# Kernel tuning notes

Hardware: AMD Instinct MI355X
Metric: run time of the kernel (lower is better)

Reference implementation:

```python
import jax, jax.numpy as jnp
import numpy as np

LEAKY_SLOPE = 0.2
LN_EPS = 1e-5


def _gat_layer(x, W, attn, concat):
    # x: (N, in_dim), W: (in_dim, H*D), attn: (H, 2*D)
    N = x.shape[0]
    H, two_d = attn.shape
    D = two_d // 2
    Wx = (x @ W).reshape(N, H, D)
    # (cat([src, tgt]) * attn).sum(-1) decomposes exactly into src/tgt dot products
    e_src = jnp.einsum('nhd,hd->nh', Wx, attn[:, :D])   # score contribution of node i
    e_tgt = jnp.einsum('nhd,hd->nh', Wx, attn[:, D:])   # score contribution of node j
    e = jax.nn.leaky_relu(e_src[:, None, :] + e_tgt[None, :, :], LEAKY_SLOPE)  # (N, N, H)
    a = jax.nn.softmax(e, axis=1)  # softmax over neighbors j (dropout is identity at eval)
    out = jnp.einsum('ijh,jhd->ihd', a, Wx)  # (N, H, D)
    if concat:
        return out.reshape(N, H * D)
    return out.mean(axis=1)


def reference(x, W1, attn1, W2, attn2, gamma, beta):
    h = jax.nn.elu(_gat_layer(x, W1, attn1, True))    # (N, hidden)
    h = jax.nn.elu(_gat_layer(h, W2, attn2, False))   # (N, hidden)
    mu = jnp.mean(h, axis=-1, keepdims=True)
    var = jnp.var(h, axis=-1, keepdims=True)
    return gamma * (h - mu) * jax.lax.rsqrt(var + LN_EPS) + beta


def setup_inputs() -> dict:
    key = jax.random.key(0)
    ks = jax.random.split(key, 5)
    N, state_dim, hidden, H = 4096, 128, 256, 4
    d0 = hidden // H  # 64, layer-0 per-head dim
    x = jax.random.normal(ks[0], (N, state_dim), dtype=jnp.float32)
    W1 = jax.random.normal(ks[1], (state_dim, H * d0), dtype=jnp.float32) / np.sqrt(state_dim)
    attn1 = jax.random.normal(ks[2], (H, 2 * d0), dtype=jnp.float32) / np.sqrt(2 * d0)
    W2 = jax.random.normal(ks[3], (hidden, H * hidden), dtype=jnp.float32) / np.sqrt(hidden)
    attn2 = jax.random.normal(ks[4], (H, 2 * hidden), dtype=jnp.float32) / np.sqrt(2 * hidden)
    gamma = jnp.ones((hidden,), dtype=jnp.float32)
    beta = jnp.zeros((hidden,), dtype=jnp.float32)
    return {"x": x, "W1": W1, "attn1": attn1, "W2": W2, "attn2": attn2,
            "gamma": gamma, "beta": beta}
```

## Files before the change

### kernel.cpp

```cpp
#include <hip/hip_runtime.h>
#include <math.h>

#define NND 4096
#define SDIM 128
#define HEADS 4
#define D1 64
#define HID 256
#define D2 256
#define C2 1024
#define NP1 (NND + 1)
#define CH 512
#define CHR 8
#define LEAKY 0.2f
#define LN_EPS 1e-5f

typedef __attribute__((ext_vector_type(8))) short bf16x8;
typedef __attribute__((ext_vector_type(4))) float f32x4;
typedef __attribute__((ext_vector_type(8))) unsigned short u16x8;

__device__ __forceinline__ unsigned short f2bf(float f) {
    union { float f; unsigned u; } v; v.f = f;
    unsigned r = v.u + 0x7FFFu + ((v.u >> 16) & 1u);
    return (unsigned short)(r >> 16);
}
__device__ __forceinline__ float bf2f(unsigned short s) {
    union { unsigned u; float f; } v; v.u = ((unsigned)s) << 16; return v.f;
}
__device__ __forceinline__ float wave_sum(float v) {
#pragma unroll
    for (int o = 32; o > 0; o >>= 1) v += __shfl_xor(v, o, 64);
    return v;
}
__device__ __forceinline__ int lower_bound_f(const float* __restrict__ a, float x) {
    int lo = 0, hi = NND;
    while (lo < hi) {
        int mid = (lo + hi) >> 1;
        if (a[mid] < x) lo = mid + 1; else hi = mid;
    }
    return lo;
}
__device__ __forceinline__ int chunk_of(int row, int kg) {
    return ((row >> 4) << 6) + (kg << 4) + (row & 15);
}

#define MM(a, b, c) c = __builtin_amdgcn_mfma_f32_16x16x32_bf16(a, b, c, 0, 0, 0)

__device__ __forceinline__ void sort_block(unsigned* key, int* pr,
        const float* __restrict__ et,
        float* __restrict__ ts, int* __restrict__ perm, int h, int e0, int t) {
    for (int p = t; p < NND; p += 256) {
        unsigned u = __float_as_uint(et[h * NND + p]);
        key[p] = (u & 0x80000000u) ? ~u : (u | 0x80000000u);
    }
    if (t < 64) pr[t] = 0;
    __syncthreads();
    const int e = t & 63, sg = t >> 6;
    const int myIdx = e0 + e;
    const unsigned myU = key[myIdx];
    int rank = 0;
    const int kbeg = sg * (NND / 4);
    for (int kb = kbeg; kb < kbeg + NND / 4; kb += 16) {
        uint4 v0 = *(const uint4*)&key[kb];
        uint4 v1 = *(const uint4*)&key[kb + 4];
        uint4 v2 = *(const uint4*)&key[kb + 8];
        uint4 v3 = *(const uint4*)&key[kb + 12];
        unsigned vv[16] = {v0.x, v0.y, v0.z, v0.w, v1.x, v1.y, v1.z, v1.w,
                           v2.x, v2.y, v2.z, v2.w, v3.x, v3.y, v3.z, v3.w};
#pragma unroll
        for (int q = 0; q < 16; q++) {
            unsigned v = vv[q];
            rank += (int)(v < myU) + (int)((v == myU) & ((kb + q) < myIdx));
        }
    }
    atomicAdd(&pr[e], rank);
    __syncthreads();
    if (t < 64) {
        int r = pr[t];
        unsigned u = key[e0 + t];
        float f = (u & 0x80000000u) ? __uint_as_float(u ^ 0x80000000u)
                                    : __uint_as_float(~u);
        ts[h * NND + r] = f;
        perm[h * NND + r] = e0 + t;
    }
}

__device__ __forceinline__ void wprep_block(const float* __restrict__ ts,
        float* __restrict__ SA, float* __restrict__ SB, int h, int t,
        float* swA, float* swB) {
    const int lane = t & 63, w = t >> 6;
    const float tmax = ts[h * NND + NND - 1];
    float a[16], b[16];
    float la = 0.f, lb = 0.f;
    const int kb = t * 16;
#pragma unroll
    for (int q = 0; q < 16; q++) {
        float u = ts[h * NND + kb + q] - tmax;
        a[q] = expf(u); b[q] = expf(LEAKY * u);
        la += a[q]; lb += b[q];
    }
    float sa = la, sb = lb;
#pragma unroll
    for (int o = 1; o < 64; o <<= 1) {
        float ua = __shfl_up(sa, o, 64);
        float ub = __shfl_up(sb, o, 64);
        if (lane >= o) { sa += ua; sb += ub; }
    }
    if (lane == 63) { swA[w] = sa; swB[w] = sb; }
    __syncthreads();
    float baseA = 0.f, baseB = 0.f, totA = 0.f, totB = 0.f;
#pragma unroll
    for (int ww = 0; ww < 4; ww++) {
        float va = swA[ww], vb = swB[ww];
        totA += va; totB += vb;
        if (ww < w) { baseA += va; baseB += vb; }
    }
    float preA = baseA + sa - la;
    float preB = baseB + sb - lb;
#pragma unroll
    for (int q = 0; q < 16; q++) {
        SA[h * NP1 + kb + q] = totA - preA;
        SB[h * NP1 + kb + q] = preB;
        preA += a[q]; preB += b[q];
    }
    if (t == 255) { SA[h * NP1 + NND] = 0.f; SB[h * NP1 + NND] = totB; }
}

__global__ __launch_bounds__(256) void k1_gemm1_prep(
        const float* __restrict__ x, const float* __restrict__ W1,
        const float* __restrict__ attn1,
        const float* __restrict__ W2, const float* __restrict__ attn2,
        float* __restrict__ Wx1, float* __restrict__ es1, float* __restrict__ et1,
        unsigned short* __restrict__ W2h, unsigned short* __restrict__ W2l,
        float* __restrict__ w_es, float* __restrict__ w_et) {
    union SM1 {
        struct {
            unsigned short Ah[256][8], Al[256][8], Bh[256][8], Bl[256][8];
            float esP[2][2][32], etP[2][2][32];
        } g;
        float tile[64][65];
    };
    __shared__ SM1 sm;
    const int bid = blockIdx.x, t = threadIdx.x;
    if (bid < 256) {
        const int lane = t & 63, w = t >> 6;
        const int wm = w >> 1, wn = w & 1;
        const int h = bid & 3, n0 = h * 64, m0 = (bid >> 2) * 64;
        const int fr = lane & 15, kg = lane >> 4;
        const int srow = t & 63, skg = t >> 6;
        const int sc = chunk_of(srow, skg);
        f32x4 z4 = {0.f, 0.f, 0.f, 0.f};
        f32x4 acc[2][2] = {{z4, z4}, {z4, z4}};
        for (int k0 = 0; k0 < SDIM; k0 += 32) {
            {
                float fv[8];
                *(float4*)&fv[0] = *(const float4*)&x[(size_t)(m0 + srow) * SDIM + k0 + skg * 8];
                *(float4*)&fv[4] = *(const float4*)&x[(size_t)(m0 + srow) * SDIM + k0 + skg * 8 + 4];
                u16x8 ph, pl;
#pragma unroll
                for (int i = 0; i < 8; i++) {
                    unsigned short hi = f2bf(fv[i]);
                    ph[i] = hi; pl[i] = f2bf(fv[i] - bf2f(hi));
                }
                *(u16x8*)&sm.g.Ah[sc][0] = ph;
                *(u16x8*)&sm.g.Al[sc][0] = pl;
            }
            {
                u16x8 ph, pl;
#pragma unroll
                for (int i = 0; i < 8; i++) {
                    float v = W1[(size_t)(k0 + skg * 8 + i) * HID + n0 + srow];
                    unsigned short hi = f2bf(v);
                    ph[i] = hi; pl[i] = f2bf(v - bf2f(hi));
                }
                *(u16x8*)&sm.g.Bh[sc][0] = ph;
                *(u16x8*)&sm.g.Bl[sc][0] = pl;
            }
            __syncthreads();
            bf16x8 ah0 = *(bf16x8*)&sm.g.Ah[wm * 128 + lane][0];
            bf16x8 ah1 = *(bf16x8*)&sm.g.Ah[wm * 128 + 64 + lane][0];
            bf16x8 al0 = *(bf16x8*)&sm.g.Al[wm * 128 + lane][0];
            bf16x8 al1 = *(bf16x8*)&sm.g.Al[wm * 128 + 64 + lane][0];
            bf16x8 bh0 = *(bf16x8*)&sm.g.Bh[wn * 128 + lane][0];
            bf16x8 bh1 = *(bf16x8*)&sm.g.Bh[wn * 128 + 64 + lane][0];
            bf16x8 bl0 = *(bf16x8*)&sm.g.Bl[wn * 128 + lane][0];
            bf16x8 bl1 = *(bf16x8*)&sm.g.Bl[wn * 128 + 64 + lane][0];
            MM(ah0, bh0, acc[0][0]); MM(ah0, bl0, acc[0][0]); MM(al0, bh0, acc[0][0]);
            MM(ah0, bh1, acc[0][1]); MM(ah0, bl1, acc[0][1]); MM(al0, bh1, acc[0][1]);
            MM(ah1, bh0, acc[1][0]); MM(ah1, bl0, acc[1][0]); MM(al1, bh0, acc[1][0]);
            MM(ah1, bh1, acc[1][1]); MM(ah1, bl1, acc[1][1]); MM(al1, bh1, acc[1][1]);
            __syncthreads();
        }
        const float as0 = attn1[h * 128 + wn * 32 + fr];
        const float as1 = attn1[h * 128 + wn * 32 + 16 + fr];
        const float at0 = attn1[h * 128 + 64 + wn * 32 + fr];
        const float at1 = attn1[h * 128 + 64 + wn * 32 + 16 + fr];
#pragma unroll
        for (int mb = 0; mb < 2; mb++) {
#pragma unroll
            for (int r = 0; r < 4; r++) {
                int row = m0 + wm * 32 + mb * 16 + kg * 4 + r;
#pragma unroll
                for (int nb = 0; nb < 2; nb++)
                    Wx1[(size_t)row * HID + n0 + wn * 32 + nb * 16 + fr] = acc[mb][nb][r];
                float ve = acc[mb][0][r] * as0 + acc[mb][1][r] * as1;
                float vt = acc[mb][0][r] * at0 + acc[mb][1][r] * at1;
#pragma unroll
                for (int msk = 1; msk < 16; msk <<= 1) {
                    ve += __shfl_xor(ve, msk, 64);
                    vt += __shfl_xor(vt, msk, 64);
                }
                if (fr == 0) {
                    sm.g.esP[wm][wn][mb * 16 + kg * 4 + r] = ve;
                    sm.g.etP[wm][wn][mb * 16 + kg * 4 + r] = vt;
                }
            }
        }
        __syncthreads();
        if (t < 64) {
            int wmm = t >> 5, ri = t & 31;
            es1[h * NND + m0 + t] = sm.g.esP[wmm][0][ri] + sm.g.esP[wmm][1][ri];
            et1[h * NND + m0 + t] = sm.g.etP[wmm][0][ri] + sm.g.etP[wmm][1][ri];
        }
    } else if (bid < 320) {
        const int tb = bid - 256;
        const int tk = tb & 3, tn = tb >> 2;
#pragma unroll
        for (int q = 0; q < 16; q++) {
            int idx = q * 256 + t;
            int kr = idx >> 6, nc = idx & 63;
            sm.tile[kr][nc] = W2[(size_t)(tk * 64 + kr) * C2 + tn * 64 + nc];
        }
        __syncthreads();
#pragma unroll
        for (int q = 0; q < 16; q++) {
            int idx = q * 256 + t;
            int nr = idx >> 6, kc = idx & 63;
            float v = sm.tile[kc][nr];
            unsigned short hi = f2bf(v);
            size_t o = (size_t)(tn * 64 + nr) * HID + tk * 64 + kc;
            W2h[o] = hi;
            W2l[o] = f2bf(v - bf2f(hi));
        }
    } else {
        int g = (bid - 320) * 4 + (t >> 6);
        int lane = t & 63;
        int k = g & 255, hs = g >> 8, h = hs >> 1, sel = hs & 1;
        float acc = 0.f;
#pragma unroll
        for (int qq = 0; qq < 4; qq++)
            acc += W2[(size_t)k * C2 + h * 256 + qq * 64 + lane] *
                   attn2[h * 512 + sel * 256 + qq * 64 + lane];
        acc = wave_sum(acc);
        if (lane == 0) {
            if (sel) w_et[h * 256 + k] = acc;
            else     w_es[h * 256 + k] = acc;
        }
    }
}

__global__ __launch_bounds__(256) void k2_sort(const float* __restrict__ et,
        float* __restrict__ ts, int* __restrict__ perm) {
    __shared__ unsigned key[NND];
    __shared__ int pr[64];
    const int bid = blockIdx.x, t = threadIdx.x;
    sort_block(key, pr, et, ts, perm, bid >> 6, (bid & 63) * 64, t);
}

__global__ __launch_bounds__(256) void k3_scan1_p1(const float* __restrict__ Wx1,
        const float* __restrict__ ts1, const int* __restrict__ perm1,
        float* __restrict__ cTA, float* __restrict__ cTB,
        float* __restrict__ SA, float* __restrict__ SB) {
    __shared__ float swA[4], swB[4];
    const int bid = blockIdx.x, t = threadIdx.x;
    if (bid >= CH) { wprep_block(ts1, SA, SB, bid - CH, t, swA, swB); return; }
    const int h = t >> 6, d = t & 63;
    const int k0 = bid * CHR;
    const float tmax = ts1[h * NND + NND - 1];
    float aA = 0.f, aB = 0.f;
#pragma unroll
    for (int r = 0; r < CHR; r++) {
        float u = ts1[h * NND + k0 + r] - tmax;
        float wa = expf(u), wb = expf(LEAKY * u);
        int j = perm1[h * NND + k0 + r];
        float v = Wx1[(size_t)j * HID + h * D1 + d];
        aA += wa * v; aB += wb * v;
    }
    cTA[(h * CH + bid) * D1 + d] = aA;
    cTB[(h * CH + bid) * D1 + d] = aB;
}

__global__ __launch_bounds__(256) void k_scan_p2(float* __restrict__ cTA,
        float* __restrict__ cTB, float* __restrict__ TotA, float* __restrict__ TotB,
        int logD) {
    const int t = threadIdx.x;
    const int lane = t & 63, w = t >> 6;
    const int D = 1 << logD;
    const int col = blockIdx.x * 4 + w;
    const int h = col >> logD, d = col & (D - 1);
    const size_t base = (size_t)h * CH * D + d;
    float vA[8], vB[8];
#pragma unroll
    for (int q = 0; q < 8; q++) {
        size_t o = base + (size_t)(lane * 8 + q) * D;
        vA[q] = cTA[o];
        vB[q] = cTB[o];
    }
    float laA = 0.f, laB = 0.f;
#pragma unroll
    for (int q = 0; q < 8; q++) { laA += vA[q]; laB += vB[q]; }
    float sA = laA, sB = laB;
#pragma unroll
    for (int o = 1; o < 64; o <<= 1) {
        float uA = __shfl_up(sA, o, 64);
        float uB = __shfl_up(sB, o, 64);
        if (lane >= o) { sA += uA; sB += uB; }
    }
    float totA = __shfl(sA, 63, 64);
    float totB = __shfl(sB, 63, 64);
    float runA = sA - laA, runB = sB - laB;
#pragma unroll
    for (int q = 0; q < 8; q++) {
        size_t o = base + (size_t)(lane * 8 + q) * D;
        float tA = vA[q], tB = vB[q];
        cTA[o] = runA;
        cTB[o] = runB;
        runA += tA; runB += tB;
    }
    if (lane == 0) {
        TotA[h * D + d] = totA;
        TotB[h * D + d] = totB;
    }
}

__global__ __launch_bounds__(256) void k5_scan1_p3(const float* __restrict__ Wx1,
        const float* __restrict__ ts1, const int* __restrict__ perm1,
        const float* __restrict__ cTA, const float* __restrict__ cTB,
        const float* __restrict__ TotA,
        float* __restrict__ A, float* __restrict__ B) {
    const int ch = blockIdx.x, t = threadIdx.x;
    const int h = t >> 6, d = t & 63;
    const float tmax = ts1[h * NND + NND - 1];
    float runA = cTA[(h * CH + ch) * D1 + d];
    float runB = cTB[(h * CH + ch) * D1 + d];
    const float totA = TotA[h * D1 + d];
    const int k0 = ch * CHR;
    float v[CHR], wa[CHR], wb[CHR];
#pragma unroll
    for (int r = 0; r < CHR; r++) {
        float u = ts1[h * NND + k0 + r] - tmax;
        wa[r] = expf(u); wb[r] = expf(LEAKY * u);
        int j = perm1[h * NND + k0 + r];
        v[r] = Wx1[(size_t)j * HID + h * D1 + d];
    }
#pragma unroll
    for (int r = 0; r < CHR; r++) {
        size_t o = ((size_t)(h * NP1 + k0 + r)) * D1 + d;
        A[o] = totA - runA;
        B[o] = runB;
        runA += wa[r] * v[r];
        runB += wb[r] * v[r];
    }
    if (ch == CH - 1) {
        size_t o = ((size_t)(h * NP1 + NND)) * D1 + d;
        A[o] = totA - runA;
        B[o] = runB;
    }
}

__global__ __launch_bounds__(256) void k6_lookup1(const float* __restrict__ es,
        const float* __restrict__ ts,
        const float* __restrict__ A, const float* __restrict__ Bv,
        const float* __restrict__ SA, const float* __restrict__ SB,
        const float* __restrict__ w_es, const float* __restrict__ w_et,
        unsigned short* __restrict__ h1h, unsigned short* __restrict__ h1l,
        float* __restrict__ es2, float* __restrict__ et2) {
    __shared__ float hbuf[256];
    const int i = blockIdx.x, t = threadIdx.x;
    const int h = t >> 6, d = t & 63;
    const int lane = t & 63, wid = t >> 6;
    float c = es[h * NND + i];
    float tmax = ts[h * NND + NND - 1];
    float s = c + tmax;
    float m = (s >= 0.f) ? s : LEAKY * s;
    float al = expf(s - m);
    float be = expf(LEAKY * s - m);
    int k = lower_bound_f(ts + h * NND, -c);
    size_t o = ((size_t)(h * NP1 + k)) * D1 + d;
    float num = al * A[o] + be * Bv[o];
    float den = al * SA[h * NP1 + k] + be * SB[h * NP1 + k];
    float val = num / den;
    float hv = (val > 0.f) ? val : expm1f(val);
    unsigned short hh = f2bf(hv);
    h1h[i * HID + t] = hh;
    h1l[i * HID + t] = f2bf(hv - bf2f(hh));
    hbuf[t] = hv;
    __syncthreads();
    float4 hv4 = *(const float4*)&hbuf[lane * 4];
    float4 we4 = *(const float4*)&w_es[wid * HID + lane * 4];
    float4 wt4 = *(const float4*)&w_et[wid * HID + lane * 4];
    float pes = hv4.x * we4.x + hv4.y * we4.y + hv4.z * we4.z + hv4.w * we4.w;
    float pet = hv4.x * wt4.x + hv4.y * wt4.y + hv4.z * wt4.z + hv4.w * wt4.w;
    pes = wave_sum(pes);
    pet = wave_sum(pet);
    if (lane == 0) {
        es2[wid * NND + i] = pes;
        et2[wid * NND + i] = pet;
    }
}

__global__ __launch_bounds__(256) void k7_gemm2_sort2(
        const unsigned short* __restrict__ h1h, const unsigned short* __restrict__ h1l,
        const unsigned short* __restrict__ W2h, const unsigned short* __restrict__ W2l,
        float* __restrict__ Wx2,
        const float* __restrict__ et2, float* __restrict__ ts2, int* __restrict__ perm2) {
    union SM7 {
        struct { unsigned short Ah[512][8], Al[512][8], Bh[256][8], Bl[256][8]; } g;
        struct { unsigned key[NND]; int pr[64]; } s;
    };
    __shared__ SM7 sm;
    const int bid = blockIdx.x, t = threadIdx.x;
    if (bid >= 512) {
        sort_block(sm.s.key, sm.s.pr, et2, ts2, perm2,
                   (bid - 512) >> 6, ((bid - 512) & 63) * 64, t);
        return;
    }
    const int lane = t & 63, w = t >> 6;
    const int n0 = (bid & 15) * 64, m0 = (bid >> 4) * 128;
    const int fr = lane & 15, kg = lane >> 4;
    const int srow = t & 63, skg = t >> 6;
    f32x4 z4 = {0.f, 0.f, 0.f, 0.f};
    f32x4 acc[2][4] = {{z4, z4, z4, z4}, {z4, z4, z4, z4}};
    u16x8 rAh[2], rAl[2], rBh, rBl;
    auto load_step = [&](int k0) {
#pragma unroll
        for (int rr = 0; rr < 2; rr++) {
            rAh[rr] = *(const u16x8*)&h1h[(size_t)(m0 + rr * 64 + srow) * HID + k0 + skg * 8];
            rAl[rr] = *(const u16x8*)&h1l[(size_t)(m0 + rr * 64 + srow) * HID + k0 + skg * 8];
        }
        rBh = *(const u16x8*)&W2h[(size_t)(n0 + srow) * HID + k0 + skg * 8];
        rBl = *(const u16x8*)&W2l[(size_t)(n0 + srow) * HID + k0 + skg * 8];
    };
    load_step(0);
    for (int k0 = 0; k0 < HID; k0 += 32) {
#pragma unroll
        for (int rr = 0; rr < 2; rr++) {
            int c = chunk_of(rr * 64 + srow, skg);
            *(u16x8*)&sm.g.Ah[c][0] = rAh[rr];
            *(u16x8*)&sm.g.Al[c][0] = rAl[rr];
        }
        int cb = chunk_of(srow, skg);
        *(u16x8*)&sm.g.Bh[cb][0] = rBh;
        *(u16x8*)&sm.g.Bl[cb][0] = rBl;
        __syncthreads();
        if (k0 + 32 < HID) load_step(k0 + 32);
        bf16x8 ah[2], al[2], bh[4], bl[4];
#pragma unroll
        for (int mb = 0; mb < 2; mb++) {
            ah[mb] = *(bf16x8*)&sm.g.Ah[w * 128 + mb * 64 + lane][0];
            al[mb] = *(bf16x8*)&sm.g.Al[w * 128 + mb * 64 + lane][0];
        }
#pragma unroll
        for (int nb = 0; nb < 4; nb++) {
            bh[nb] = *(bf16x8*)&sm.g.Bh[nb * 64 + lane][0];
            bl[nb] = *(bf16x8*)&sm.g.Bl[nb * 64 + lane][0];
        }
#pragma unroll
        for (int mb = 0; mb < 2; mb++)
#pragma unroll
            for (int nb = 0; nb < 4; nb++) {
                MM(ah[mb], bh[nb], acc[mb][nb]);
                MM(ah[mb], bl[nb], acc[mb][nb]);
                MM(al[mb], bh[nb], acc[mb][nb]);
            }
        __syncthreads();
    }
#pragma unroll
    for (int mb = 0; mb < 2; mb++)
#pragma unroll
        for (int r = 0; r < 4; r++) {
            int row = m0 + w * 32 + mb * 16 + kg * 4 + r;
#pragma unroll
            for (int nb = 0; nb < 4; nb++)
                Wx2[(size_t)row * C2 + n0 + nb * 16 + fr] = acc[mb][nb][r];
        }
}

__global__ __launch_bounds__(256) void k8_scan2_p1(const float* __restrict__ Wx2,
        const float* __restrict__ ts2, const int* __restrict__ perm2,
        float* __restrict__ cTA, float* __restrict__ cTB,
        float* __restrict__ SA, float* __restrict__ SB) {
    __shared__ float swA[4], swB[4];
    const int bid = blockIdx.x, t = threadIdx.x;
    if (bid >= 2048) { wprep_block(ts2, SA, SB, bid - 2048, t, swA, swB); return; }
    const int ch = bid & (CH - 1), h = bid >> 9;
    const int d = t, k0 = ch * CHR;
    const float tmax = ts2[h * NND + NND - 1];
    float aA = 0.f, aB = 0.f;
#pragma unroll
    for (int r = 0; r < CHR; r++) {
        float u = ts2[h * NND + k0 + r] - tmax;
        float wa = expf(u), wb = expf(LEAKY * u);
        int j = perm2[h * NND + k0 + r];
        float v = Wx2[(size_t)j * C2 + h * D2 + d];
        aA += wa * v; aB += wb * v;
    }
    cTA[(h * CH + ch) * D2 + d] = aA;
    cTB[(h * CH + ch) * D2 + d] = aB;
}

__global__ __launch_bounds__(256) void k10_scan2_p3(const float* __restrict__ Wx2,
        const float* __restrict__ ts2, const int* __restrict__ perm2,
        const float* __restrict__ cTA, const float* __restrict__ cTB,
        const float* __restrict__ TotA,
        float* __restrict__ A, float* __restrict__ B) {
    const int bid = blockIdx.x, t = threadIdx.x;
    const int ch = bid & (CH - 1), h = bid >> 9;
    const int d = t;
    const float tmax = ts2[h * NND + NND - 1];
    float runA = cTA[(h * CH + ch) * D2 + d];
    float runB = cTB[(h * CH + ch) * D2 + d];
    const float totA = TotA[h * D2 + d];
    const int k0 = ch * CHR;
    float v[CHR], wa[CHR], wb[CHR];
#pragma unroll
    for (int r = 0; r < CHR; r++) {
        float u = ts2[h * NND + k0 + r] - tmax;
        wa[r] = expf(u); wb[r] = expf(LEAKY * u);
        int j = perm2[h * NND + k0 + r];
        v[r] = Wx2[(size_t)j * C2 + h * D2 + d];
    }
#pragma unroll
    for (int r = 0; r < CHR; r++) {
        size_t o = ((size_t)(h * NP1 + k0 + r)) * D2 + d;
        A[o] = totA - runA;
        B[o] = runB;
        runA += wa[r] * v[r];
        runB += wb[r] * v[r];
    }
    if (ch == CH - 1) {
        size_t o = ((size_t)(h * NP1 + NND)) * D2 + d;
        A[o] = totA - runA;
        B[o] = runB;
    }
}

__global__ __launch_bounds__(256) void k11_lookup2(const float* __restrict__ es,
        const float* __restrict__ ts,
        const float* __restrict__ A, const float* __restrict__ B,
        const float* __restrict__ SA, const float* __restrict__ SB,
        const float* __restrict__ gamma, const float* __restrict__ betap,
        float* __restrict__ out) {
    __shared__ float red[4];
    const int i = blockIdx.x;
    const int t = threadIdx.x;
    const int wid = t >> 6, lane = t & 63;
    float acc = 0.f;
#pragma unroll
    for (int h = 0; h < HEADS; h++) {
        float c = es[h * NND + i];
        float tmax = ts[h * NND + NND - 1];
        float s = c + tmax;
        float m = (s >= 0.f) ? s : LEAKY * s;
        float al = expf(s - m);
        float be = expf(LEAKY * s - m);
        int k = lower_bound_f(ts + h * NND, -c);
        size_t o = ((size_t)(h * NP1 + k)) * D2 + t;
        float num = al * A[o] + be * B[o];
        float den = al * SA[h * NP1 + k] + be * SB[h * NP1 + k];
        acc += num / den;
    }
    acc *= 0.25f;
    float xv = (acc > 0.f) ? acc : expm1f(acc);
    float sv = wave_sum(xv);
    if (lane == 0) red[wid] = sv;
    __syncthreads();
    float mu = (red[0] + red[1] + red[2] + red[3]) * (1.f / 256.f);
    __syncthreads();
    float dv = xv - mu;
    float s2 = wave_sum(dv * dv);
    if (lane == 0) red[wid] = s2;
    __syncthreads();
    float var = (red[0] + red[1] + red[2] + red[3]) * (1.f / 256.f);
    out[i * D2 + t] = gamma[t] * dv * rsqrtf(var + LN_EPS) + betap[t];
}

extern "C" void kernel_launch(void* const* d_in, const int* in_sizes, int n_in,
                              void* d_out, int out_size, void* d_ws, size_t ws_size,
                              hipStream_t stream) {
    const float* x     = (const float*)d_in[0];
    const float* W1    = (const float*)d_in[1];
    const float* attn1 = (const float*)d_in[2];
    const float* W2    = (const float*)d_in[3];
    const float* attn2 = (const float*)d_in[4];
    const float* gamma = (const float*)d_in[5];
    const float* betap = (const float*)d_in[6];
    float* out = (float*)d_out;

    char* ws = (char*)d_ws;
    size_t off = 0;
    auto alloc = [&](size_t nbytes) -> void* {
        void* p = (void*)(ws + off);
        off += (nbytes + 255) & ~(size_t)255;
        return p;
    };

    float* Wx1 = (float*)alloc((size_t)NND * HID * 4);
    float* Wx2 = (float*)alloc((size_t)NND * C2 * 4);
    unsigned short* h1h = (unsigned short*)alloc((size_t)NND * HID * 2);
    unsigned short* h1l = (unsigned short*)alloc((size_t)NND * HID * 2);
    float* es1 = (float*)alloc((size_t)HEADS * NND * 4);
    float* et1 = (float*)alloc((size_t)HEADS * NND * 4);
    float* es2 = (float*)alloc((size_t)HEADS * NND * 4);
    float* et2 = (float*)alloc((size_t)HEADS * NND * 4);
    float* ts1 = (float*)alloc((size_t)HEADS * NND * 4);
    float* ts2 = (float*)alloc((size_t)HEADS * NND * 4);
    int* perm1 = (int*)alloc((size_t)HEADS * NND * 4);
    int* perm2 = (int*)alloc((size_t)HEADS * NND * 4);
    float* A   = (float*)alloc((size_t)HEADS * NP1 * D2 * 4);
    float* B   = (float*)alloc((size_t)HEADS * NP1 * D2 * 4);
    float* SA  = (float*)alloc((size_t)HEADS * NP1 * 4);
    float* SB  = (float*)alloc((size_t)HEADS * NP1 * 4);
    float* cTA = (float*)alloc((size_t)HEADS * CH * D2 * 4);
    float* cTB = (float*)alloc((size_t)HEADS * CH * D2 * 4);
    float* TotA = (float*)alloc((size_t)HEADS * D2 * 4);
    float* TotB = (float*)alloc((size_t)HEADS * D2 * 4);
    unsigned short* W2h = (unsigned short*)alloc((size_t)262144 * 2);
    unsigned short* W2l = (unsigned short*)alloc((size_t)262144 * 2);
    float* w_es = (float*)alloc((size_t)HEADS * HID * 4);
    float* w_et = (float*)alloc((size_t)HEADS * HID * 4);
    (void)ws_size; (void)in_sizes; (void)n_in; (void)out_size;

    k1_gemm1_prep<<<832, 256, 0, stream>>>(x, W1, attn1, W2, attn2,
                                           Wx1, es1, et1, W2h, W2l, w_es, w_et);
    k2_sort<<<256, 256, 0, stream>>>(et1, ts1, perm1);
    k3_scan1_p1<<<CH + 4, 256, 0, stream>>>(Wx1, ts1, perm1, cTA, cTB, SA, SB);
    k_scan_p2<<<64, 256, 0, stream>>>(cTA, cTB, TotA, TotB, 6);
    k5_scan1_p3<<<CH, 256, 0, stream>>>(Wx1, ts1, perm1, cTA, cTB, TotA, A, B);
    k6_lookup1<<<NND, 256, 0, stream>>>(es1, ts1, A, B, SA, SB, w_es, w_et,
                                        h1h, h1l, es2, et2);

    k7_gemm2_sort2<<<768, 256, 0, stream>>>(h1h, h1l, W2h, W2l, Wx2, et2, ts2, perm2);
    k8_scan2_p1<<<2052, 256, 0, stream>>>(Wx2, ts2, perm2, cTA, cTB, SA, SB);
    k_scan_p2<<<256, 256, 0, stream>>>(cTA, cTB, TotA, TotB, 8);
    k10_scan2_p3<<<2048, 256, 0, stream>>>(Wx2, ts2, perm2, cTA, cTB, TotA, A, B);
    k11_lookup2<<<NND, 256, 0, stream>>>(es2, ts2, A, B, SA, SB, gamma, betap, out);
}
```

Before: 167.7 us.

## Use single bf16 GEMM2 with k-group-packed operand layouts

The second GEMM (h1 @ W2) drops the split-bf16 hi/lo scheme and runs a single bf16 MFMA per tile, cutting MFMA count to a third. The h1 and W2 operands are now written in a k-group-major packed layout, so the loads and LDS stores are contiguous and need no swizzle. The GEMM1 A-tile staging mapping is also changed to read x rows more contiguously. The cost is lower precision in Wx2, which feeds a softmax-weighted aggregation and layernorm and could exceed the tolerance.

```diff
diff --git a/kernel.cpp b/kernel.cpp
--- a/kernel.cpp
+++ b/kernel.cpp
@@ -130,7 +130,7 @@
         const float* __restrict__ attn1,
         const float* __restrict__ W2, const float* __restrict__ attn2,
         float* __restrict__ Wx1, float* __restrict__ es1, float* __restrict__ et1,
-        unsigned short* __restrict__ W2h, unsigned short* __restrict__ W2l,
+        unsigned short* __restrict__ W2p,
         float* __restrict__ w_es, float* __restrict__ w_et) {
     union SM1 {
         struct {
@@ -146,34 +146,36 @@
         const int wm = w >> 1, wn = w & 1;
         const int h = bid & 3, n0 = h * 64, m0 = (bid >> 2) * 64;
         const int fr = lane & 15, kg = lane >> 4;
-        const int srow = t & 63, skg = t >> 6;
-        const int sc = chunk_of(srow, skg);
+        const int arow = t >> 2, akg = t & 3;
+        const int ac = chunk_of(arow, akg);
+        const int brow = t & 63, bkg = t >> 6;
+        const int bc = chunk_of(brow, bkg);
         f32x4 z4 = {0.f, 0.f, 0.f, 0.f};
         f32x4 acc[2][2] = {{z4, z4}, {z4, z4}};
         for (int k0 = 0; k0 < SDIM; k0 += 32) {
             {
                 float fv[8];
-                *(float4*)&fv[0] = *(const float4*)&x[(size_t)(m0 + srow) * SDIM + k0 + skg * 8];
-                *(float4*)&fv[4] = *(const float4*)&x[(size_t)(m0 + srow) * SDIM + k0 + skg * 8 + 4];
+                *(float4*)&fv[0] = *(const float4*)&x[(size_t)(m0 + arow) * SDIM + k0 + akg * 8];
+                *(float4*)&fv[4] = *(const float4*)&x[(size_t)(m0 + arow) * SDIM + k0 + akg * 8 + 4];
                 u16x8 ph, pl;
 #pragma unroll
                 for (int i = 0; i < 8; i++) {
                     unsigned short hi = f2bf(fv[i]);
                     ph[i] = hi; pl[i] = f2bf(fv[i] - bf2f(hi));
                 }
-                *(u16x8*)&sm.g.Ah[sc][0] = ph;
-                *(u16x8*)&sm.g.Al[sc][0] = pl;
+                *(u16x8*)&sm.g.Ah[ac][0] = ph;
+                *(u16x8*)&sm.g.Al[ac][0] = pl;
             }
             {
                 u16x8 ph, pl;
 #pragma unroll
                 for (int i = 0; i < 8; i++) {
-                    float v = W1[(size_t)(k0 + skg * 8 + i) * HID + n0 + srow];
+                    float v = W1[(size_t)(k0 + bkg * 8 + i) * HID + n0 + brow];
                     unsigned short hi = f2bf(v);
                     ph[i] = hi; pl[i] = f2bf(v - bf2f(hi));
                 }
-                *(u16x8*)&sm.g.Bh[sc][0] = ph;
-                *(u16x8*)&sm.g.Bl[sc][0] = pl;
+                *(u16x8*)&sm.g.Bh[bc][0] = ph;
+                *(u16x8*)&sm.g.Bl[bc][0] = pl;
             }
             __syncthreads();
             bf16x8 ah0 = *(bf16x8*)&sm.g.Ah[wm * 128 + lane][0];
@@ -236,10 +238,9 @@
             int idx = q * 256 + t;
             int nr = idx >> 6, kc = idx & 63;
             float v = sm.tile[kc][nr];
-            unsigned short hi = f2bf(v);
-            size_t o = (size_t)(tn * 64 + nr) * HID + tk * 64 + kc;
-            W2h[o] = hi;
-            W2l[o] = f2bf(v - bf2f(hi));
+            int kglob = tk * 64 + kc;
+            size_t o = ((size_t)(kglob >> 3) * C2 + tn * 64 + nr) * 8 + (kglob & 7);
+            W2p[o] = f2bf(v);
         }
     } else {
         int g = (bid - 320) * 4 + (t >> 6);
@@ -372,7 +373,7 @@
         const float* __restrict__ A, const float* __restrict__ Bv,
         const float* __restrict__ SA, const float* __restrict__ SB,
         const float* __restrict__ w_es, const float* __restrict__ w_et,
-        unsigned short* __restrict__ h1h, unsigned short* __restrict__ h1l,
+        unsigned short* __restrict__ h1p,
         float* __restrict__ es2, float* __restrict__ et2) {
     __shared__ float hbuf[256];
     const int i = blockIdx.x, t = threadIdx.x;
@@ -390,9 +391,7 @@
     float den = al * SA[h * NP1 + k] + be * SB[h * NP1 + k];
     float val = num / den;
     float hv = (val > 0.f) ? val : expm1f(val);
-    unsigned short hh = f2bf(hv);
-    h1h[i * HID + t] = hh;
-    h1l[i * HID + t] = f2bf(hv - bf2f(hh));
+    h1p[((size_t)(t >> 3) * NND + i) * 8 + (t & 7)] = f2bf(hv);
     hbuf[t] = hv;
     __syncthreads();
     float4 hv4 = *(const float4*)&hbuf[lane * 4];
@@ -409,12 +408,11 @@
 }
 
 __global__ __launch_bounds__(256) void k7_gemm2_sort2(
-        const unsigned short* __restrict__ h1h, const unsigned short* __restrict__ h1l,
-        const unsigned short* __restrict__ W2h, const unsigned short* __restrict__ W2l,
+        const unsigned short* __restrict__ h1p, const unsigned short* __restrict__ W2p,
         float* __restrict__ Wx2,
         const float* __restrict__ et2, float* __restrict__ ts2, int* __restrict__ perm2) {
     union SM7 {
-        struct { unsigned short Ah[512][8], Al[512][8], Bh[256][8], Bl[256][8]; } g;
+        struct { unsigned short Ah[512][8], Bh[256][8]; } g;
         struct { unsigned key[NND]; int pr[64]; } s;
     };
     __shared__ SM7 sm;
@@ -427,51 +425,36 @@
     const int lane = t & 63, w = t >> 6;
     const int n0 = (bid & 15) * 64, m0 = (bid >> 4) * 128;
     const int fr = lane & 15, kg = lane >> 4;
-    const int srow = t & 63, skg = t >> 6;
     f32x4 z4 = {0.f, 0.f, 0.f, 0.f};
     f32x4 acc[2][4] = {{z4, z4, z4, z4}, {z4, z4, z4, z4}};
-    u16x8 rAh[2], rAl[2], rBh, rBl;
+    u16x8 rA[2], rB;
     auto load_step = [&](int k0) {
-#pragma unroll
-        for (int rr = 0; rr < 2; rr++) {
-            rAh[rr] = *(const u16x8*)&h1h[(size_t)(m0 + rr * 64 + srow) * HID + k0 + skg * 8];
-            rAl[rr] = *(const u16x8*)&h1l[(size_t)(m0 + rr * 64 + srow) * HID + k0 + skg * 8];
-        }
-        rBh = *(const u16x8*)&W2h[(size_t)(n0 + srow) * HID + k0 + skg * 8];
-        rBl = *(const u16x8*)&W2l[(size_t)(n0 + srow) * HID + k0 + skg * 8];
+        int kgrp = (k0 >> 3) + w;
+#pragma unroll
+        for (int rr = 0; rr < 2; rr++)
+            rA[rr] = *(const u16x8*)&h1p[((size_t)kgrp * NND + m0 + rr * 64 + lane) * 8];
+        rB = *(const u16x8*)&W2p[((size_t)kgrp * C2 + n0 + lane) * 8];
     };
     load_step(0);
     for (int k0 = 0; k0 < HID; k0 += 32) {
 #pragma unroll
-        for (int rr = 0; rr < 2; rr++) {
-            int c = chunk_of(rr * 64 + srow, skg);
-            *(u16x8*)&sm.g.Ah[c][0] = rAh[rr];
-            *(u16x8*)&sm.g.Al[c][0] = rAl[rr];
-        }
-        int cb = chunk_of(srow, skg);
-        *(u16x8*)&sm.g.Bh[cb][0] = rBh;
-        *(u16x8*)&sm.g.Bl[cb][0] = rBl;
+        for (int rr = 0; rr < 2; rr++)
+            *(u16x8*)&sm.g.Ah[w * 128 + rr * 64 + lane][0] = rA[rr];
+        *(u16x8*)&sm.g.Bh[w * 64 + lane][0] = rB;
         __syncthreads();
         if (k0 + 32 < HID) load_step(k0 + 32);
-        bf16x8 ah[2], al[2], bh[4], bl[4];
-#pragma unroll
-        for (int mb = 0; mb < 2; mb++) {
-            ah[mb] = *(bf16x8*)&sm.g.Ah[w * 128 + mb * 64 + lane][0];
-            al[mb] = *(bf16x8*)&sm.g.Al[w * 128 + mb * 64 + lane][0];
-        }
-#pragma unroll
-        for (int nb = 0; nb < 4; nb++) {
-            bh[nb] = *(bf16x8*)&sm.g.Bh[nb * 64 + lane][0];
-            bl[nb] = *(bf16x8*)&sm.g.Bl[nb * 64 + lane][0];
-        }
+        bf16x8 ah[2], bh[4];
 #pragma unroll
         for (int mb = 0; mb < 2; mb++)
-#pragma unroll
-            for (int nb = 0; nb < 4; nb++) {
+            ah[mb] = *(bf16x8*)&sm.g.Ah[kg * 128 + w * 32 + mb * 16 + fr][0];
+#pragma unroll
+        for (int nb = 0; nb < 4; nb++)
+            bh[nb] = *(bf16x8*)&sm.g.Bh[kg * 64 + nb * 16 + fr][0];
+#pragma unroll
+        for (int mb = 0; mb < 2; mb++)
+#pragma unroll
+            for (int nb = 0; nb < 4; nb++)
                 MM(ah[mb], bh[nb], acc[mb][nb]);
-                MM(ah[mb], bl[nb], acc[mb][nb]);
-                MM(al[mb], bh[nb], acc[mb][nb]);
-            }
         __syncthreads();
     }
 #pragma unroll
@@ -606,8 +589,7 @@
 
     float* Wx1 = (float*)alloc((size_t)NND * HID * 4);
     float* Wx2 = (float*)alloc((size_t)NND * C2 * 4);
-    unsigned short* h1h = (unsigned short*)alloc((size_t)NND * HID * 2);
-    unsigned short* h1l = (unsigned short*)alloc((size_t)NND * HID * 2);
+    unsigned short* h1p = (unsigned short*)alloc((size_t)NND * HID * 2);
     float* es1 = (float*)alloc((size_t)HEADS * NND * 4);
     float* et1 = (float*)alloc((size_t)HEADS * NND * 4);
     float* es2 = (float*)alloc((size_t)HEADS * NND * 4);
@@ -624,22 +606,21 @@
     float* cTB = (float*)alloc((size_t)HEADS * CH * D2 * 4);
     float* TotA = (float*)alloc((size_t)HEADS * D2 * 4);
     float* TotB = (float*)alloc((size_t)HEADS * D2 * 4);
-    unsigned short* W2h = (unsigned short*)alloc((size_t)262144 * 2);
-    unsigned short* W2l = (unsigned short*)alloc((size_t)262144 * 2);
+    unsigned short* W2p = (unsigned short*)alloc((size_t)262144 * 2);
     float* w_es = (float*)alloc((size_t)HEADS * HID * 4);
     float* w_et = (float*)alloc((size_t)HEADS * HID * 4);
     (void)ws_size; (void)in_sizes; (void)n_in; (void)out_size;
 
     k1_gemm1_prep<<<832, 256, 0, stream>>>(x, W1, attn1, W2, attn2,
-                                           Wx1, es1, et1, W2h, W2l, w_es, w_et);
+                                           Wx1, es1, et1, W2p, w_es, w_et);
     k2_sort<<<256, 256, 0, stream>>>(et1, ts1, perm1);
     k3_scan1_p1<<<CH + 4, 256, 0, stream>>>(Wx1, ts1, perm1, cTA, cTB, SA, SB);
     k_scan_p2<<<64, 256, 0, stream>>>(cTA, cTB, TotA, TotB, 6);
     k5_scan1_p3<<<CH, 256, 0, stream>>>(Wx1, ts1, perm1, cTA, cTB, TotA, A, B);
     k6_lookup1<<<NND, 256, 0, stream>>>(es1, ts1, A, B, SA, SB, w_es, w_et,
-                                        h1h, h1l, es2, et2);
-
-    k7_gemm2_sort2<<<768, 256, 0, stream>>>(h1h, h1l, W2h, W2l, Wx2, et2, ts2, perm2);
+                                        h1p, es2, et2);
+
+    k7_gemm2_sort2<<<768, 256, 0, stream>>>(h1p, W2p, Wx2, et2, ts2, perm2);
     k8_scan2_p1<<<2052, 256, 0, stream>>>(Wx2, ts2, perm2, cTA, cTB, SA, SB);
     k_scan_p2<<<256, 256, 0, stream>>>(cTA, cTB, TotA, TotB, 8);
     k10_scan2_p3<<<2048, 256, 0, stream>>>(Wx2, ts2, perm2, cTA, cTB, TotA, A, B);
```

Result: faster. 155.8 us (-7.1%).
